# Kernel optimization log

Measured on AMD Instinct MI355X. Metric: run time of the kernel, lower is better.

## Reference

```python
import jax, jax.numpy as jnp
import numpy as np

K = 16          # k_neighbours
BIG = 1e9       # distance penalty for masked senders


def setup_inputs() -> dict:
    key = jax.random.key(0)
    ks = jax.random.split(key, 8)
    B, N, F, H, FO = 64, 512, 64, 128, 64
    nodes = jax.random.normal(ks[0], (B, N, F), jnp.float32)
    mask = jax.random.randint(ks[1], (B, N), 0, 2, jnp.int32)

    def w(k_, sh):
        return jax.random.normal(k_, sh, jnp.float32) * (1.0 / np.sqrt(sh[0]).astype(np.float32))

    We1 = w(ks[2], (2 * F, H)); be1 = jnp.zeros((H,), jnp.float32)
    We2 = w(ks[3], (H, H));     be2 = jnp.zeros((H,), jnp.float32)
    Wn1 = w(ks[4], (F + H, H)); bn1 = jnp.zeros((H,), jnp.float32)
    Wn2 = w(ks[5], (H, FO));    bn2 = jnp.zeros((FO,), jnp.float32)
    return dict(nodes=nodes, mask=mask, We1=We1, be1=be1, We2=We2, be2=be2,
                Wn1=Wn1, bn1=bn1, Wn2=Wn2, bn2=bn2)


def reference(nodes, mask, We1, be1, We2, be2, Wn1, bn1, Wn2, bn2):
    # nodes: [B,N,F] ; mask: [B,N] (1 = real node, 0 = padding)
    m = mask.astype(nodes.dtype)                      # [B,N]
    x = nodes * m[..., None]                          # zero padded nodes

    # --- dynamic kNN graph (euclidean_squared + top_k, no self connection) ---
    sq = jnp.sum(x * x, axis=-1)                      # [B,N]
    dist = jnp.abs(sq[:, :, None] + sq[:, None, :]
                   - 2.0 * jnp.einsum('bnf,bmf->bnm', x, x))  # [B,N,N]
    dist = dist + BIG * (1.0 - m)[:, None, :]         # never select masked senders
    _, idx = jax.lax.top_k(-dist, K + 1)              # [B,N,K+1]
    idx = idx[..., 1:]                                # drop self connection -> [B,N,K]

    # --- gather sender features / masks along edges ---
    gathered = jax.vmap(lambda xf, ib: xf[ib])(x, idx)    # [B,N,K,F]
    smask = jax.vmap(lambda mv, ib: mv[ib])(m, idx)       # [B,N,K]
    recv = jnp.broadcast_to(x[:, :, None, :], gathered.shape)
    edges = jnp.concatenate([recv, gathered], axis=-1)    # [B,N,K,2F] ('concat' aggregation)

    # --- edge MLP (gather-compute) ---
    h = jax.nn.relu(edges @ We1 + be1)
    h = jax.nn.relu(h @ We2 + be2)                        # [B,N,K,H]

    # --- masked mean pooling over edges (scatter back to nodes) ---
    emask = m[:, :, None] * smask                         # edge valid iff both endpoints valid
    h = h * emask[..., None]
    cnt = jnp.maximum(jnp.sum(emask, axis=-1, keepdims=True), 1.0)  # [B,N,1]
    pooled = jnp.sum(h, axis=2) / cnt                     # [B,N,H]

    # --- node update MLP ---
    nh = jnp.concatenate([x, pooled], axis=-1)            # [B,N,F+H]
    out = jax.nn.relu(nh @ Wn1 + bn1) @ Wn2 + bn2         # [B,N,FO]
    return out * m[..., None]                             # zero padded nodes in output
```

## Files before the change

### kernel.cpp

```cpp
#include <hip/hip_runtime.h>

#define DI __device__ __forceinline__

typedef __bf16 bf16_t;
typedef __bf16 bf16x4 __attribute__((ext_vector_type(4)));
typedef __bf16 bf16x8 __attribute__((ext_vector_type(8)));
typedef float f32x4 __attribute__((ext_vector_type(4)));
typedef unsigned long long u64;


DI bf16_t f2b(float f) {
  unsigned u = __float_as_uint(f);
  unsigned r = (u + 0x7fffu + ((u >> 16) & 1u)) >> 16;
  return __builtin_bit_cast(bf16_t, (unsigned short)r);
}
DI float b2f(bf16_t h) {
  return __uint_as_float(((unsigned)__builtin_bit_cast(unsigned short, h)) << 16);
}
DI f32x4 zero4() { f32x4 z = {0.f, 0.f, 0.f, 0.f}; return z; }

DI bf16x8 make_frag(const float* p, bool wantlo) {
  float4 v0 = *(const float4*)p;
  float4 v1 = *(const float4*)(p + 4);
  float vv[8] = {v0.x, v0.y, v0.z, v0.w, v1.x, v1.y, v1.z, v1.w};
  bf16x8 a;
#pragma unroll
  for (int j = 0; j < 8; ++j) {
    bf16_t hi = f2b(vv[j]);
    a[j] = wantlo ? f2b(vv[j] - b2f(hi)) : hi;
  }
  return a;
}
DI void make_frag2(const float* p, bf16x8* hi, bf16x8* lo) {
  float4 v0 = *(const float4*)p;
  float4 v1 = *(const float4*)(p + 4);
  float vv[8] = {v0.x, v0.y, v0.z, v0.w, v1.x, v1.y, v1.z, v1.w};
#pragma unroll
  for (int j = 0; j < 8; ++j) {
    bf16_t h = f2b(vv[j]);
    (*hi)[j] = h;
    (*lo)[j] = f2b(vv[j] - b2f(h));
  }
}

DI u64 u64min(u64 a, u64 b) { return a < b ? a : b; }
template <int CTRL>
DI u64 dpp_u64(u64 v) {
  int lo = (int)(unsigned)(v & 0xffffffffull);
  int hi = (int)(unsigned)(v >> 32);
  int tlo = __builtin_amdgcn_update_dpp(0, lo, CTRL, 0xF, 0xF, true);
  int thi = __builtin_amdgcn_update_dpp(0, hi, CTRL, 0xF, 0xF, true);
  return (((u64)(unsigned)thi) << 32) | (unsigned)tlo;
}
template <int CTRL>
DI float dpp_f32(float v) {
  int t = __builtin_amdgcn_update_dpp(0, (int)__float_as_uint(v), CTRL, 0xF, 0xF, true);
  return __uint_as_float((unsigned)t);
}
DI u64 rowmin_u64(u64 v) {
  v = u64min(v, dpp_u64<0xB1>(v));
  v = u64min(v, dpp_u64<0x4E>(v));
  v = u64min(v, dpp_u64<0x141>(v));
  v = u64min(v, dpp_u64<0x140>(v));
  return v;
}
DI float rowsum_f32(float v) {
  v += dpp_f32<0xB1>(v);
  v += dpp_f32<0x4E>(v);
  v += dpp_f32<0x141>(v);
  v += dpp_f32<0x140>(v);
  return v;
}
DI void bitonic16(u64* a) {
#pragma unroll
  for (int k = 2; k <= 16; k <<= 1)
#pragma unroll
    for (int j = k >> 1; j > 0; j >>= 1)
#pragma unroll
      for (int i = 0; i < 16; ++i) {
        const int l = i ^ j;
        if (l > i) {
          const bool up = ((i & k) == 0);
          const bool sw = up ? (a[i] > a[l]) : (a[i] < a[l]);
          const u64 t0 = a[i], t1 = a[l];
          a[i] = sw ? t1 : t0;
          a[l] = sw ? t0 : t1;
        }
      }
}
DI void sorted_insert16(u64* a, u64 k) {
  u64 na[16];
#pragma unroll
  for (int p = 0; p < 16; ++p) {
    const bool cur_gt = (a[p] > k);
    const bool prv_le = (p == 0) ? true : (a[p - 1] <= k);
    na[p] = !cur_gt ? a[p] : (prv_le ? k : a[p - 1]);
  }
#pragma unroll
  for (int p = 0; p < 16; ++p) a[p] = na[p];
}

__global__ void __launch_bounds__(256) kfuse(const float* __restrict__ nodes,
    const int* __restrict__ mask,
    const float* __restrict__ We1, const float* __restrict__ We2,
    const float* __restrict__ Wn1, const float* __restrict__ Wn2,
    float* __restrict__ x, bf16_t* __restrict__ xhi, bf16_t* __restrict__ xlo,
    float* __restrict__ sq, int* __restrict__ vlist, int* __restrict__ vcnt,
    bf16_t* __restrict__ W1p, bf16_t* __restrict__ W2p,
    bf16_t* __restrict__ Wn1p, bf16_t* __restrict__ Wn2p) {
  const int blk = blockIdx.x, t = threadIdx.x;
  __shared__ int cnts[8];
  __shared__ int basep[8];

  if (blk < 512) {
    const int b = blk >> 3, n0 = (blk & 7) * 64;
#pragma unroll
    for (int i = 0; i < 4; ++i) {
      const int idx = t + 256 * i;
      const int gi = b * 512 + n0 + (idx >> 4);
      const int fo = (idx & 15) * 4;
      const float fm = (float)mask[gi];
      const size_t ro = (size_t)gi * 64;
      float4 v = *(const float4*)(nodes + ro + fo);
      v.x *= fm; v.y *= fm; v.z *= fm; v.w *= fm;
      *(float4*)(x + ro + fo) = v;
      float vv[4] = {v.x, v.y, v.z, v.w};
      bf16x4 hh, ll;
#pragma unroll
      for (int k = 0; k < 4; ++k) {
        bf16_t hi = f2b(vv[k]);
        hh[k] = hi;
        ll[k] = f2b(vv[k] - b2f(hi));
      }
      *(bf16x4*)(xhi + ro + fo) = hh;
      *(bf16x4*)(xlo + ro + fo) = ll;
      float s = v.x * v.x + v.y * v.y + v.z * v.z + v.w * v.w;
      s = rowsum_f32(s);
      if ((t & 15) == 0) sq[gi] = s;
    }
  } else if (blk < 576) {
    const int b = blk - 512, lane = t & 63, w = t >> 6;
    unsigned long long bal[2]; int flag[2];
#pragma unroll
    for (int h = 0; h < 2; ++h) {
      flag[h] = (mask[b * 512 + h * 256 + t] != 0);
      bal[h] = __ballot(flag[h]);
      if (lane == 0) cnts[h * 4 + w] = __popcll(bal[h]);
    }
    __syncthreads();
    if (t == 0) {
      int a = 0;
      for (int c = 0; c < 8; ++c) { basep[c] = a; a += cnts[c]; }
      vcnt[b] = a;
    }
    __syncthreads();
#pragma unroll
    for (int h = 0; h < 2; ++h) {
      if (flag[h]) {
        const unsigned long long lt = (lane == 0) ? 0ull : (~0ull >> (64 - lane));
        const int pos = basep[h * 4 + w] + __popcll(bal[h] & lt);
        vlist[b * 512 + pos] = h * 256 + t;
      }
    }
  } else {
    int p = (blk - 576) * 256 + t;
    const float* W; bf16_t* dst; int K, Nn, local, mode;
    if (p < 4096)       { W = We1; dst = W1p;  K = 128; Nn = 128; mode = 0; local = p; }
    else if (p < 8192)  { W = We2; dst = W2p;  K = 128; Nn = 128; mode = 1; local = p - 4096; }
    else if (p < 14336) { W = Wn1; dst = Wn1p; K = 192; Nn = 128; mode = 0; local = p - 8192; }
    else                { W = Wn2; dst = Wn2p; K = 128; Nn = 64;  mode = 1; local = p - 14336; }
    int lane = local & 63;
    int nnt = (Nn >> 4);
    int chunk = local >> 6;
    int nt = chunk % nnt;
    int s = chunk / nnt;
    int n = nt * 16 + (lane & 15);
    int kbase = s * 32 + ((lane >> 4) * 8);
    bf16x8 v;
#pragma unroll
    for (int j = 0; j < 8; ++j) {
      int kp = kbase + j;
      int region = kp / K;
      int kk = kp - region * K;
      float w = W[kk * Nn + n];
      bf16_t hi = f2b(w);
      v[j] = (mode == 1 && region == 1) ? f2b(w - b2f(hi)) : hi;
    }
    *(bf16x8*)(dst + (size_t)local * 8) = v;
  }
}

__global__ void __launch_bounds__(256) kknn(const bf16_t* __restrict__ xhi,
    const bf16_t* __restrict__ xlo,
    const float* __restrict__ sq, const int* __restrict__ vlist,
    const int* __restrict__ vcnt, int* __restrict__ idxg) {
  const int b = blockIdx.x & 63, tile = blockIdx.x >> 6;
  const int nv = vcnt[b];
  if (tile * 16 >= nv) return;
  const int t = threadIdx.x, lane = t & 63, w = t >> 6;
  const int i = lane >> 4, d = lane & 15;
  __shared__ float sqs[512];
  __shared__ int vls[512];
  __shared__ __align__(16) float S[16 * 520];
  for (int k = t; k < 512; k += 256) { sqs[k] = sq[b * 512 + k]; vls[k] = vlist[b * 512 + k]; }
  __syncthreads();

  const size_t xb = (size_t)b * 512 * 64;

  const int aslot = tile * 16 + d;
  const int arow = vls[aslot < nv ? aslot : 0];
  bf16x8 ah[2], al[2];
#pragma unroll
  for (int kh = 0; kh < 2; ++kh) {
    ah[kh] = *(const bf16x8*)(xhi + xb + (size_t)arow * 64 + kh * 32 + i * 8);
    al[kh] = *(const bf16x8*)(xlo + xb + (size_t)arow * 64 + kh * 32 + i * 8);
  }

  const int rslot = tile * 16 + w * 4 + i;
  const bool vrow = (rslot < nv);
  const int nrow = vls[rslot < nv ? rslot : 0];
  const float sqn = sqs[nrow];

  int crs[8];
#pragma unroll
  for (int jj = 0; jj < 8; ++jj) {
    const int c = (w + 4 * jj) * 16 + d;
    crs[jj] = vls[c < nv ? c : 0];
  }

  bf16x8 bh[2], bl[2];
  if (w * 16 < nv) {
#pragma unroll
    for (int kh = 0; kh < 2; ++kh) {
      bh[kh] = *(const bf16x8*)(xhi + xb + (size_t)crs[0] * 64 + kh * 32 + i * 8);
      bl[kh] = *(const bf16x8*)(xlo + xb + (size_t)crs[0] * 64 + kh * 32 + i * 8);
    }
  }
  for (int jj = 0; jj < 8; ++jj) {
    const int ct = w + 4 * jj;
    if (ct * 16 >= nv) break;
    bf16x8 nbh[2], nbl[2];
    const bool pre = (jj < 7) && ((w + 4 * (jj + 1)) * 16 < nv);
    if (pre) {
#pragma unroll
      for (int kh = 0; kh < 2; ++kh) {
        nbh[kh] = *(const bf16x8*)(xhi + xb + (size_t)crs[jj + 1] * 64 + kh * 32 + i * 8);
        nbl[kh] = *(const bf16x8*)(xlo + xb + (size_t)crs[jj + 1] * 64 + kh * 32 + i * 8);
      }
    }
    f32x4 acc = zero4();
#pragma unroll
    for (int kh = 0; kh < 2; ++kh) {
      acc = __builtin_amdgcn_mfma_f32_16x16x32_bf16(ah[kh], bh[kh], acc, 0, 0, 0);
      acc = __builtin_amdgcn_mfma_f32_16x16x32_bf16(ah[kh], bl[kh], acc, 0, 0, 0);
      acc = __builtin_amdgcn_mfma_f32_16x16x32_bf16(al[kh], bh[kh], acc, 0, 0, 0);
      acc = __builtin_amdgcn_mfma_f32_16x16x32_bf16(al[kh], bl[kh], acc, 0, 0, 0);
    }
#pragma unroll
    for (int r = 0; r < 4; ++r) S[(i * 4 + r) * 520 + ct * 16 + d] = acc[r];
    if (pre) {
#pragma unroll
      for (int kh = 0; kh < 2; ++kh) { bh[kh] = nbh[kh]; bl[kh] = nbl[kh]; }
    }
  }
  __syncthreads();

  const u64 INF64 = ~0ull;
  u64 s1[16];
#pragma unroll
  for (int j = 0; j < 16; ++j) s1[j] = INF64;
#pragma unroll
  for (int j = 0; j < 16; ++j) {
    if (j * 16 < nv) {
      const int c = j * 16 + d;
      const int m = vls[c < nv ? c : 0];
      const float dot = S[(w * 4 + i) * 520 + j * 16 + d];
      const float dd = fabsf(sqn + sqs[m] - 2.f * dot);
      const u64 key = (((u64)__float_as_uint(dd)) << 32) | (unsigned)m;
      const bool ok = (c < nv) && (m != nrow);
      s1[j] = ok ? key : INF64;
    }
  }
  bitonic16(s1);
  for (int j = 16; j * 16 < nv; ++j) {
    const int c = j * 16 + d;
    const int m = vls[c < nv ? c : 0];
    const float dot = S[(w * 4 + i) * 520 + j * 16 + d];
    const float dd = fabsf(sqn + sqs[m] - 2.f * dot);
    const u64 key = (((u64)__float_as_uint(dd)) << 32) | (unsigned)m;
    const bool ok = (c < nv) && (m != nrow);
    sorted_insert16(s1, ok ? key : INF64);
  }

  int res = nrow;
#pragma unroll
  for (int ts = 0; ts < 16; ++ts) {
    const u64 wmin = rowmin_u64(s1[0]);
    if (d == ts) res = (wmin == INF64) ? nrow : (int)(unsigned)(wmin & 0xffffffffull);
    const bool w1 = (wmin != INF64) && (s1[0] == wmin);
#pragma unroll
    for (int k = 0; k < 15; ++k) s1[k] = w1 ? s1[k + 1] : s1[k];
    s1[15] = w1 ? INF64 : s1[15];
  }
  if (vrow) idxg[((size_t)b * 512 + rslot) * 16 + d] = res;
}

__global__ void __launch_bounds__(256, 2) kedge(const bf16_t* __restrict__ xhi,
    const bf16_t* __restrict__ xlo, const int* __restrict__ idxg,
    const int* __restrict__ vlist, const int* __restrict__ vcnt,
    const bf16_t* __restrict__ W1p, const bf16_t* __restrict__ W2p,
    const float* __restrict__ be1, const float* __restrict__ be2,
    float* __restrict__ pooled) {
  __shared__ __align__(16) bf16_t wbuf[32768];
  __shared__ __align__(16) bf16_t hfrag[4][2][1024];
  const int t = threadIdx.x, lane = t & 63, w = t >> 6;
  const int q = lane >> 4, e = lane & 15;
  const int bb = blockIdx.x & 63;
  const int s0 = ((blockIdx.x >> 6) * 4 + w) * 2;

  {
    const uint4* s1 = (const uint4*)W1p;
    const uint4* s2 = (const uint4*)W2p;
    uint4* dst = (uint4*)wbuf;
#pragma unroll
    for (int i = 0; i < 8; ++i) dst[t + 256 * i] = s1[t + 256 * i];
#pragma unroll
    for (int i = 0; i < 8; ++i) dst[2048 + t + 256 * i] = s2[t + 256 * i];
  }
  __syncthreads();

  const int nv = vcnt[bb];
  if (s0 >= nv) return;

  int vl[2], sv[2];
  {
#pragma unroll
    for (int u = 0; u < 2; ++u) {
      const int sl = (s0 + u) < nv ? (s0 + u) : 0;
      vl[u] = vlist[bb * 512 + sl];
      sv[u] = idxg[((size_t)(bb * 512 + sl) << 4) + e];
    }
  }

  for (int base = s0; base < nv; base += 64) {
    const bool act1 = (base + 1) < nv;
    const int gid0 = bb * 512 + vl[0];
    const int gid1 = bb * 512 + vl[1];
    const size_t rb0 = (size_t)gid0 << 6;
    const size_t rb1 = (size_t)gid1 << 6;
    const size_t nb0 = (size_t)(bb * 512 + sv[0]) << 6;
    const size_t nb1 = (size_t)(bb * 512 + sv[1]) << 6;

    bf16x8 af[2][8];
#pragma unroll
    for (int k = 0; k < 4; ++k) {
      const int off = (k & 1) * 32 + q * 8;
      const bf16_t* pl = (k >> 1) ? xlo : xhi;
      af[0][k]     = *(const bf16x8*)(pl + rb0 + off);
      af[1][k]     = *(const bf16x8*)(pl + rb1 + off);
      af[0][4 + k] = *(const bf16x8*)(pl + nb0 + off);
      af[1][4 + k] = *(const bf16x8*)(pl + nb1 + off);
    }

    int nvl[2] = {vl[0], vl[1]}, nsv[2] = {sv[0], sv[1]};
    {
      const int nb = base + 64;
      if (nb < nv) {
#pragma unroll
        for (int u = 0; u < 2; ++u) {
          const int sl = (nb + u) < nv ? (nb + u) : 0;
          nvl[u] = vlist[bb * 512 + sl];
          nsv[u] = idxg[((size_t)(bb * 512 + sl) << 4) + e];
        }
      }
    }

    f32x4 acc[2][8];
#pragma unroll
    for (int u = 0; u < 2; ++u)
#pragma unroll
      for (int nt = 0; nt < 8; ++nt) acc[u][nt] = zero4();

#pragma unroll
    for (int ph = 0; ph < 2; ++ph)
#pragma unroll
      for (int inner = 0; inner < 2; ++inner) {
        const bf16_t* wb = wbuf + (ph * 2 + inner) * 4096;
        const bf16x8 h0 = af[0][ph * 4 + inner];
        const bf16x8 h1 = af[1][ph * 4 + inner];
        const bf16x8 l0 = af[0][ph * 4 + 2 + inner];
        const bf16x8 l1 = af[1][ph * 4 + 2 + inner];
#pragma unroll
        for (int nt = 0; nt < 8; ++nt) {
          const bf16x8 bfv = *(const bf16x8*)(wb + (nt * 64 + lane) * 8);
          acc[0][nt] = __builtin_amdgcn_mfma_f32_16x16x32_bf16(h0, bfv, acc[0][nt], 0, 0, 0);
          acc[0][nt] = __builtin_amdgcn_mfma_f32_16x16x32_bf16(l0, bfv, acc[0][nt], 0, 0, 0);
          acc[1][nt] = __builtin_amdgcn_mfma_f32_16x16x32_bf16(h1, bfv, acc[1][nt], 0, 0, 0);
          acc[1][nt] = __builtin_amdgcn_mfma_f32_16x16x32_bf16(l1, bfv, acc[1][nt], 0, 0, 0);
        }
      }

    f32x4 acc2[2][8];
#pragma unroll
    for (int u = 0; u < 2; ++u)
#pragma unroll
      for (int nt = 0; nt < 8; ++nt) acc2[u][nt] = zero4();

#pragma unroll
    for (int hh = 0; hh < 2; ++hh) {
#pragma unroll
      for (int u = 0; u < 2; ++u)
#pragma unroll
        for (int nt4 = 0; nt4 < 4; ++nt4) {
          const int nt = hh * 4 + nt4;
          const int cc = nt * 16 + e;
          const float bv = be1[cc];
          const int bse = (((cc >> 5) & 1) * 64 + q * 4 + 16 * ((cc >> 3) & 3)) * 8 + (cc & 7);
#pragma unroll
          for (int r = 0; r < 4; ++r)
            hfrag[w][u][bse + r * 8] = f2b(fmaxf(acc[u][nt][r] + bv, 0.f));
        }
#pragma unroll
      for (int sl = 0; sl < 2; ++sl) {
        const int f = hh * 2 + sl;
        const bf16x8 a20 = *(const bf16x8*)(&hfrag[w][0][(sl * 64 + lane) * 8]);
        const bf16x8 a21 = *(const bf16x8*)(&hfrag[w][1][(sl * 64 + lane) * 8]);
        const bf16_t* wb2 = wbuf + 16384 + f * 4096;
#pragma unroll
        for (int nt = 0; nt < 8; ++nt) {
          const bf16x8 bfv = *(const bf16x8*)(wb2 + (nt * 64 + lane) * 8);
          acc2[0][nt] = __builtin_amdgcn_mfma_f32_16x16x32_bf16(a20, bfv, acc2[0][nt], 0, 0, 0);
          acc2[1][nt] = __builtin_amdgcn_mfma_f32_16x16x32_bf16(a21, bfv, acc2[1][nt], 0, 0, 0);
        }
      }
    }

#pragma unroll
    for (int u = 0; u < 2; ++u) {
      if (u == 0 || act1) {
        const int gid = u ? gid1 : gid0;
#pragma unroll
        for (int nt = 0; nt < 8; ++nt) {
          const float bv = be2[nt * 16 + e];
          float part = 0.f;
#pragma unroll
          for (int r = 0; r < 4; ++r) part += fmaxf(acc2[u][nt][r] + bv, 0.f);
          part += __shfl_xor(part, 16, 64);
          part += __shfl_xor(part, 32, 64);
          if (lane < 16) pooled[(size_t)gid * 128 + nt * 16 + lane] = part * 0.0625f;
        }
      }
    }

    vl[0] = nvl[0]; vl[1] = nvl[1];
    sv[0] = nsv[0]; sv[1] = nsv[1];
  }
}

__global__ void __launch_bounds__(256, 2) knode(const float* __restrict__ x,
    const float* __restrict__ pooled, const int* __restrict__ mask,
    const bf16_t* __restrict__ Wn1p, const bf16_t* __restrict__ Wn2p,
    const float* __restrict__ bn1, const float* __restrict__ bn2,
    float* __restrict__ out) {
  __shared__ __align__(16) bf16_t wbuf[32768];
  __shared__ __align__(16) bf16_t hfrag[4][1024];
  const int t = threadIdx.x, lane = t & 63, w = t >> 6;
  const int q = lane >> 4, e = lane & 15;
  const int nodebase = (blockIdx.x * 4 + w) * 16;

  {
    const uint4* s1 = (const uint4*)Wn1p;
    const uint4* s2 = (const uint4*)Wn2p;
    uint4* dst = (uint4*)wbuf;
#pragma unroll
    for (int i = 0; i < 12; ++i) dst[t + 256 * i] = s1[t + 256 * i];
#pragma unroll
    for (int i = 0; i < 4; ++i) dst[3072 + t + 256 * i] = s2[t + 256 * i];
  }
  __syncthreads();

  f32x4 acc[8];
#pragma unroll
  for (int nt = 0; nt < 8; ++nt) acc[nt] = zero4();

#pragma unroll
  for (int sr = 0; sr < 6; ++sr) {
    const int col = sr * 32 + q * 8;
    const int node = nodebase + e;
    const float* p = (col < 64) ? (x + (size_t)node * 64 + col)
                                : (pooled + (size_t)node * 128 + (col - 64));
    bf16x8 afh, afl;
    make_frag2(p, &afh, &afl);
#pragma unroll
    for (int nt = 0; nt < 8; ++nt) {
      const bf16x8 bfv = *(const bf16x8*)(wbuf + sr * 4096 + (nt * 64 + lane) * 8);
      acc[nt] = __builtin_amdgcn_mfma_f32_16x16x32_bf16(afh, bfv, acc[nt], 0, 0, 0);
      acc[nt] = __builtin_amdgcn_mfma_f32_16x16x32_bf16(afl, bfv, acc[nt], 0, 0, 0);
    }
  }

  f32x4 acc2[4];
#pragma unroll
  for (int nt = 0; nt < 4; ++nt) acc2[nt] = zero4();

#pragma unroll
  for (int hh = 0; hh < 2; ++hh) {
#pragma unroll
    for (int nt4 = 0; nt4 < 4; ++nt4) {
      const int nt = hh * 4 + nt4;
      const int cc = nt * 16 + e;
      const float bv = bn1[cc];
      const int bse = (((cc >> 5) & 1) * 64 + q * 4 + 16 * ((cc >> 3) & 3)) * 8 + (cc & 7);
#pragma unroll
      for (int r = 0; r < 4; ++r)
        hfrag[w][bse + r * 8] = f2b(fmaxf(acc[nt][r] + bv, 0.f));
    }
#pragma unroll
    for (int sl = 0; sl < 2; ++sl) {
      const int f = hh * 2 + sl;
      const bf16x8 a2 = *(const bf16x8*)(&hfrag[w][(sl * 64 + lane) * 8]);
      const bf16_t* wb2 = wbuf + 24576 + f * 2048;
#pragma unroll
      for (int nt = 0; nt < 4; ++nt) {
        const bf16x8 bfv = *(const bf16x8*)(wb2 + (nt * 64 + lane) * 8);
        acc2[nt] = __builtin_amdgcn_mfma_f32_16x16x32_bf16(a2, bfv, acc2[nt], 0, 0, 0);
      }
    }
  }

  int mm[4];
#pragma unroll
  for (int r = 0; r < 4; ++r) mm[r] = mask[nodebase + q * 4 + r];
#pragma unroll
  for (int nt = 0; nt < 4; ++nt) {
    const float bv = bn2[nt * 16 + e];
#pragma unroll
    for (int r = 0; r < 4; ++r) {
      const int node = nodebase + q * 4 + r;
      out[(size_t)node * 64 + nt * 16 + e] = (acc2[nt][r] + bv) * (float)mm[r];
    }
  }
}

extern "C" void kernel_launch(void* const* d_in, const int* in_sizes, int n_in,
                              void* d_out, int out_size, void* d_ws, size_t ws_size,
                              hipStream_t stream) {
  const float* nodes = (const float*)d_in[0];
  const int*   mask  = (const int*)d_in[1];
  const float* We1   = (const float*)d_in[2];
  const float* be1   = (const float*)d_in[3];
  const float* We2   = (const float*)d_in[4];
  const float* be2   = (const float*)d_in[5];
  const float* Wn1   = (const float*)d_in[6];
  const float* bn1   = (const float*)d_in[7];
  const float* Wn2   = (const float*)d_in[8];
  const float* bn2   = (const float*)d_in[9];
  float* out = (float*)d_out;

  char* p = (char*)d_ws;
  auto alloc = [&](size_t bytes) -> char* {
    char* r = p;
    p += (bytes + 255) & ~(size_t)255;
    return r;
  };
  float*  x      = (float*)alloc((size_t)32768 * 64 * 4);
  bf16_t* xhi    = (bf16_t*)alloc((size_t)32768 * 64 * 2);
  bf16_t* xlo    = (bf16_t*)alloc((size_t)32768 * 64 * 2);
  float*  sq     = (float*)alloc((size_t)32768 * 4);
  int*    vlist  = (int*)alloc((size_t)32768 * 4);
  int*    vcnt   = (int*)alloc((size_t)64 * 4);
  int*    idxg   = (int*)alloc((size_t)32768 * 16 * 4);
  float*  pooled = (float*)alloc((size_t)32768 * 128 * 4);
  bf16_t* W1p    = (bf16_t*)alloc((size_t)8 * 8 * 64 * 8 * 2);
  bf16_t* W2p    = (bf16_t*)alloc((size_t)8 * 8 * 64 * 8 * 2);
  bf16_t* Wn1p   = (bf16_t*)alloc((size_t)12 * 8 * 64 * 8 * 2);
  bf16_t* Wn2p   = (bf16_t*)alloc((size_t)8 * 4 * 64 * 8 * 2);
  if ((size_t)(p - (char*)d_ws) > ws_size) return;

  kfuse<<<640, 256, 0, stream>>>(nodes, mask, We1, We2, Wn1, Wn2,
                                 x, xhi, xlo, sq, vlist, vcnt, W1p, W2p, Wn1p, Wn2p);
  kknn<<<2048, 256, 0, stream>>>(xhi, xlo, sq, vlist, vcnt, idxg);
  kedge<<<512, 256, 0, stream>>>(xhi, xlo, idxg, vlist, vcnt, W1p, W2p, be1, be2, pooled);
  knode<<<512, 256, 0, stream>>>(x, pooled, mask, Wn1p, Wn2p, bn1, bn2, out);
}
```

Baseline: 154.8 us.

## Stream W2 from global memory to halve edge-kernel LDS and deepen kNN prefetch

In the edge kernel, W2 is no longer staged in shared memory. Its B-fragments are read directly from global/L2, and the hfrag buffer is halved by processing the second layer in four 32-column chunks instead of two 64-column chunks. Shared memory per block drops from about 80KB to about 40KB, which should allow more blocks per CU and remove the W2 copy per block, at the cost of repeated global loads of W2 in the inner loop. The kNN kernel also replaces its one-ahead double buffer with a four-deep register prefetch of neighbour column fragments and fully unrolls the loop, which raises register pressure.

Result: slower. 176.3 us (+13.9%).

```diff
diff --git a/kernel.cpp b/kernel.cpp
--- a/kernel.cpp
+++ b/kernel.cpp
@@ -228,39 +228,41 @@
     crs[jj] = vls[c < nv ? c : 0];
   }
 
-  bf16x8 bh[2], bl[2];
-  if (w * 16 < nv) {
-#pragma unroll
-    for (int kh = 0; kh < 2; ++kh) {
-      bh[kh] = *(const bf16x8*)(xhi + xb + (size_t)crs[0] * 64 + kh * 32 + i * 8);
-      bl[kh] = *(const bf16x8*)(xlo + xb + (size_t)crs[0] * 64 + kh * 32 + i * 8);
-    }
-  }
+  bf16x8 pbh[4][2], pbl[4][2];
+#pragma unroll
+  for (int jj = 0; jj < 4; ++jj) {
+    if ((w + 4 * jj) * 16 < nv) {
+#pragma unroll
+      for (int kh = 0; kh < 2; ++kh) {
+        pbh[jj][kh] = *(const bf16x8*)(xhi + xb + (size_t)crs[jj] * 64 + kh * 32 + i * 8);
+        pbl[jj][kh] = *(const bf16x8*)(xlo + xb + (size_t)crs[jj] * 64 + kh * 32 + i * 8);
+      }
+    }
+  }
+#pragma unroll
   for (int jj = 0; jj < 8; ++jj) {
     const int ct = w + 4 * jj;
-    if (ct * 16 >= nv) break;
-    bf16x8 nbh[2], nbl[2];
-    const bool pre = (jj < 7) && ((w + 4 * (jj + 1)) * 16 < nv);
-    if (pre) {
+    if (ct * 16 < nv) {
+      const int sl = jj & 3;
+      bf16x8 bh[2] = {pbh[sl][0], pbh[sl][1]};
+      bf16x8 bl[2] = {pbl[sl][0], pbl[sl][1]};
+      if (jj < 4 && (w + 4 * (jj + 4)) * 16 < nv) {
+#pragma unroll
+        for (int kh = 0; kh < 2; ++kh) {
+          pbh[sl][kh] = *(const bf16x8*)(xhi + xb + (size_t)crs[jj + 4] * 64 + kh * 32 + i * 8);
+          pbl[sl][kh] = *(const bf16x8*)(xlo + xb + (size_t)crs[jj + 4] * 64 + kh * 32 + i * 8);
+        }
+      }
+      f32x4 acc = zero4();
 #pragma unroll
       for (int kh = 0; kh < 2; ++kh) {
-        nbh[kh] = *(const bf16x8*)(xhi + xb + (size_t)crs[jj + 1] * 64 + kh * 32 + i * 8);
-        nbl[kh] = *(const bf16x8*)(xlo + xb + (size_t)crs[jj + 1] * 64 + kh * 32 + i * 8);
-      }
-    }
-    f32x4 acc = zero4();
-#pragma unroll
-    for (int kh = 0; kh < 2; ++kh) {
-      acc = __builtin_amdgcn_mfma_f32_16x16x32_bf16(ah[kh], bh[kh], acc, 0, 0, 0);
-      acc = __builtin_amdgcn_mfma_f32_16x16x32_bf16(ah[kh], bl[kh], acc, 0, 0, 0);
-      acc = __builtin_amdgcn_mfma_f32_16x16x32_bf16(al[kh], bh[kh], acc, 0, 0, 0);
-      acc = __builtin_amdgcn_mfma_f32_16x16x32_bf16(al[kh], bl[kh], acc, 0, 0, 0);
-    }
-#pragma unroll
-    for (int r = 0; r < 4; ++r) S[(i * 4 + r) * 520 + ct * 16 + d] = acc[r];
-    if (pre) {
-#pragma unroll
-      for (int kh = 0; kh < 2; ++kh) { bh[kh] = nbh[kh]; bl[kh] = nbl[kh]; }
+        acc = __builtin_amdgcn_mfma_f32_16x16x32_bf16(ah[kh], bh[kh], acc, 0, 0, 0);
+        acc = __builtin_amdgcn_mfma_f32_16x16x32_bf16(ah[kh], bl[kh], acc, 0, 0, 0);
+        acc = __builtin_amdgcn_mfma_f32_16x16x32_bf16(al[kh], bh[kh], acc, 0, 0, 0);
+        acc = __builtin_amdgcn_mfma_f32_16x16x32_bf16(al[kh], bl[kh], acc, 0, 0, 0);
+      }
+#pragma unroll
+      for (int r = 0; r < 4; ++r) S[(i * 4 + r) * 520 + ct * 16 + d] = acc[r];
     }
   }
   __syncthreads();
@@ -311,8 +313,8 @@
     const bf16_t* __restrict__ W1p, const bf16_t* __restrict__ W2p,
     const float* __restrict__ be1, const float* __restrict__ be2,
     float* __restrict__ pooled) {
-  __shared__ __align__(16) bf16_t wbuf[32768];
-  __shared__ __align__(16) bf16_t hfrag[4][2][1024];
+  __shared__ __align__(16) bf16_t wbuf[16384];
+  __shared__ __align__(16) bf16_t hfrag[4][2][512];
   const int t = threadIdx.x, lane = t & 63, w = t >> 6;
   const int q = lane >> 4, e = lane & 15;
   const int bb = blockIdx.x & 63;
@@ -320,12 +322,9 @@
 
   {
     const uint4* s1 = (const uint4*)W1p;
-    const uint4* s2 = (const uint4*)W2p;
     uint4* dst = (uint4*)wbuf;
 #pragma unroll
     for (int i = 0; i < 8; ++i) dst[t + 256 * i] = s1[t + 256 * i];
-#pragma unroll
-    for (int i = 0; i < 8; ++i) dst[2048 + t + 256 * i] = s2[t + 256 * i];
   }
   __syncthreads();
 
@@ -333,13 +332,11 @@
   if (s0 >= nv) return;
 
   int vl[2], sv[2];
-  {
-#pragma unroll
-    for (int u = 0; u < 2; ++u) {
-      const int sl = (s0 + u) < nv ? (s0 + u) : 0;
-      vl[u] = vlist[bb * 512 + sl];
-      sv[u] = idxg[((size_t)(bb * 512 + sl) << 4) + e];
-    }
+#pragma unroll
+  for (int u = 0; u < 2; ++u) {
+    const int sl = (s0 + u) < nv ? (s0 + u) : 0;
+    vl[u] = vlist[bb * 512 + sl];
+    sv[u] = idxg[((size_t)(bb * 512 + sl) << 4) + e];
   }
 
   for (int base = s0; base < nv; base += 64) {
@@ -407,25 +404,23 @@
       for (int nt = 0; nt < 8; ++nt) acc2[u][nt] = zero4();
 
 #pragma unroll
-    for (int hh = 0; hh < 2; ++hh) {
+    for (int qq = 0; qq < 4; ++qq) {
 #pragma unroll
       for (int u = 0; u < 2; ++u)
 #pragma unroll
-        for (int nt4 = 0; nt4 < 4; ++nt4) {
-          const int nt = hh * 4 + nt4;
+        for (int nt2 = 0; nt2 < 2; ++nt2) {
+          const int nt = qq * 2 + nt2;
           const int cc = nt * 16 + e;
           const float bv = be1[cc];
-          const int bse = (((cc >> 5) & 1) * 64 + q * 4 + 16 * ((cc >> 3) & 3)) * 8 + (cc & 7);
+          const int bse = (q * 4 + 16 * ((cc >> 3) & 3)) * 8 + (cc & 7);
 #pragma unroll
           for (int r = 0; r < 4; ++r)
             hfrag[w][u][bse + r * 8] = f2b(fmaxf(acc[u][nt][r] + bv, 0.f));
         }
-#pragma unroll
-      for (int sl = 0; sl < 2; ++sl) {
-        const int f = hh * 2 + sl;
-        const bf16x8 a20 = *(const bf16x8*)(&hfrag[w][0][(sl * 64 + lane) * 8]);
-        const bf16x8 a21 = *(const bf16x8*)(&hfrag[w][1][(sl * 64 + lane) * 8]);
-        const bf16_t* wb2 = wbuf + 16384 + f * 4096;
+      {
+        const bf16x8 a20 = *(const bf16x8*)(&hfrag[w][0][lane * 8]);
+        const bf16x8 a21 = *(const bf16x8*)(&hfrag[w][1][lane * 8]);
+        const bf16_t* wb2 = W2p + qq * 4096;
 #pragma unroll
         for (int nt = 0; nt < 8; ++nt) {
           const bf16x8 bfv = *(const bf16x8*)(wb2 + (nt * 64 + lane) * 8);
```
